# Optimization experiments

Measured on AMD Instinct MI355X. Metric: run time of the kernel, lower is better.

Reference implementation:

```python
import jax, jax.numpy as jnp
import numpy as np

N_GAUSS = 2_000_000
N_VERTS = 5023
N_FACES = 9976


def _safe_normalize(x, eps=1e-20):
    return x / jnp.sqrt(jnp.clip(jnp.sum(x * x, axis=-1, keepdims=True), eps, None))


def _rotmat_to_unitquat_xyzw(R):
    # scipy/roma-style branchless rotation-matrix -> unit quaternion (xyzw)
    r00, r01, r02 = R[..., 0, 0], R[..., 0, 1], R[..., 0, 2]
    r10, r11, r12 = R[..., 1, 0], R[..., 1, 1], R[..., 1, 2]
    r20, r21, r22 = R[..., 2, 0], R[..., 2, 1], R[..., 2, 2]
    t = r00 + r11 + r22
    qx = jnp.stack([1 + r00 - r11 - r22, r10 + r01, r20 + r02, r21 - r12], -1)
    qy = jnp.stack([r10 + r01, 1 - r00 + r11 - r22, r21 + r12, r02 - r20], -1)
    qz = jnp.stack([r20 + r02, r21 + r12, 1 - r00 - r11 + r22, r10 - r01], -1)
    qw = jnp.stack([r21 - r12, r02 - r20, r10 - r01, 1 + t], -1)
    decision = jnp.stack([r00, r11, r22, t], -1)
    choice = jnp.argmax(decision, axis=-1)[..., None]
    q = jnp.where(choice == 0, qx, jnp.where(choice == 1, qy, jnp.where(choice == 2, qz, qw)))
    return q / jnp.linalg.norm(q, axis=-1, keepdims=True)


def _quat_product_xyzw(p, q):
    pv, pw = p[..., :3], p[..., 3:4]
    qv, qw = q[..., :3], q[..., 3:4]
    v = pw * qv + qw * pv + jnp.cross(pv, qv)
    w = pw * qw - jnp.sum(pv * qv, axis=-1, keepdims=True)
    return jnp.concatenate([v, w], axis=-1)


def _xyzw_to_wxyz(q):
    return jnp.concatenate([q[..., 3:4], q[..., :3]], axis=-1)


def _wxyz_to_xyzw(q):
    return jnp.concatenate([q[..., 1:4], q[..., 0:1]], axis=-1)


def setup_inputs() -> dict:
    key = jax.random.key(0)
    ks = jax.random.split(key, 9)
    return {
        'verts': jax.random.normal(ks[0], (N_VERTS, 3), jnp.float32),
        'xyz': jax.random.normal(ks[1], (N_GAUSS, 3), jnp.float32),
        'opacity_raw': jax.random.normal(ks[2], (N_GAUSS, 1), jnp.float32),
        'scaling_raw': jax.random.normal(ks[3], (N_GAUSS, 3), jnp.float32),
        'rotation_raw': jax.random.normal(ks[4], (N_GAUSS, 4), jnp.float32),
        'features_dc': jax.random.normal(ks[5], (N_GAUSS, 1, 3), jnp.float32),
        'features_rest': jax.random.normal(ks[6], (N_GAUSS, 15, 3), jnp.float32),
        'faces': jax.random.randint(ks[7], (N_FACES, 3), 0, N_VERTS, jnp.int32),
        'binding': jax.random.randint(ks[8], (N_GAUSS,), 0, N_FACES, jnp.int32),
    }


def reference(verts, xyz, opacity_raw, scaling_raw, rotation_raw, features_dc, features_rest, faces, binding):
    # ---- per-face quantities (small: F ~= 10k) ----
    tri = verts[faces]                         # [F,3,3]
    face_center = tri.mean(axis=1)             # [F,3]
    v0, v1, v2 = tri[:, 0], tri[:, 1], tri[:, 2]
    a0 = _safe_normalize(v1 - v0)
    c = jnp.cross(a0, v2 - v0)
    a1 = _safe_normalize(c)
    a2 = -_safe_normalize(jnp.cross(a1, a0))
    R = jnp.stack([a0, a1, a2], axis=-1)       # [F,3,3], columns = tangent frame
    s0 = jnp.linalg.norm(v1 - v0, axis=-1, keepdims=True)
    s1 = jnp.abs(jnp.sum(c * a1, axis=-1, keepdims=True))
    face_scaling = (s0 + s1) / 2               # [F,1]
    face_quat_wxyz = _xyzw_to_wxyz(_rotmat_to_unitquat_xyzw(R))  # [F,4]

    # ---- per-Gaussian hot path: gather + 3x3 matvec + quat compose ----
    Rb = R[binding]                            # [N,3,3]
    fs = face_scaling[binding]                 # [N,1]
    g_xyz = jnp.einsum('nij,nj->ni', Rb, xyz) * fs + face_center[binding]  # [N,3]
    opacity = jax.nn.sigmoid(opacity_raw)      # [N,1]
    scales = jnp.exp(scaling_raw) * fs         # [N,3]
    rot = rotation_raw / (jnp.sqrt(jnp.sum(rotation_raw ** 2, axis=1, keepdims=True)) + 1e-12)
    fq = face_quat_wxyz[binding]
    fq = fq / (jnp.sqrt(jnp.sum(fq ** 2, axis=1, keepdims=True)) + 1e-12)
    rotations = _xyzw_to_wxyz(_quat_product_xyzw(_wxyz_to_xyzw(fq), _wxyz_to_xyzw(rot)))
    # shs = cat(features_dc, features_rest)[:, 0] == features_dc[:, 0]
    shs0 = features_dc[:, 0, :]
    color = jnp.clip(jnp.concatenate([0.5 + 0.282 * shs0, opacity], axis=-1) * 255.0, 0.0, 255.0)
    rotations = rotations / jnp.linalg.norm(rotations, axis=-1, keepdims=True)
    return jnp.concatenate([g_xyz, scales, color, rotations], axis=-1)  # [N,14]


if __name__ == '__main__':
    out = reference(**setup_inputs())
    print(out.shape, out.dtype)
```

## Files before the change

### kernel.cpp

```cpp
#include <hip/hip_runtime.h>
#include <math.h>


struct F3 { float x, y, z; };
__device__ __forceinline__ F3 mkf3(float x, float y, float z) { F3 r; r.x = x; r.y = y; r.z = z; return r; }
__device__ __forceinline__ F3 f3sub(F3 a, F3 b) { return mkf3(a.x - b.x, a.y - b.y, a.z - b.z); }
__device__ __forceinline__ F3 f3add(F3 a, F3 b) { return mkf3(a.x + b.x, a.y + b.y, a.z + b.z); }
__device__ __forceinline__ F3 f3scl(F3 a, float s) { return mkf3(a.x * s, a.y * s, a.z * s); }
__device__ __forceinline__ float f3dot(F3 a, F3 b) { return a.x * b.x + a.y * b.y + a.z * b.z; }
__device__ __forceinline__ F3 f3cross(F3 a, F3 b) {
    return mkf3(a.y * b.z - a.z * b.y, a.z * b.x - a.x * b.z, a.x * b.y - a.y * b.x);
}

__device__ void face_geom(const float* __restrict__ verts, const int* __restrict__ faces, int f,
                          F3& a0, F3& a1, F3& a2, F3& ctr, float& fs, float4& quat_wxyz)
{
    int i0 = faces[3 * f + 0], i1 = faces[3 * f + 1], i2 = faces[3 * f + 2];
    F3 v0 = mkf3(verts[3 * i0], verts[3 * i0 + 1], verts[3 * i0 + 2]);
    F3 v1 = mkf3(verts[3 * i1], verts[3 * i1 + 1], verts[3 * i1 + 2]);
    F3 v2 = mkf3(verts[3 * i2], verts[3 * i2 + 1], verts[3 * i2 + 2]);

    ctr = f3scl(f3add(f3add(v0, v1), v2), (1.0f / 3.0f));

    F3 e1 = f3sub(v1, v0);
    float d1 = f3dot(e1, e1);
    float s0 = sqrtf(d1);
    a0 = f3scl(e1, 1.0f / sqrtf(fmaxf(d1, 1e-20f)));

    F3 e2 = f3sub(v2, v0);
    F3 c = f3cross(a0, e2);
    float dc = f3dot(c, c);
    a1 = f3scl(c, 1.0f / sqrtf(fmaxf(dc, 1e-20f)));

    F3 c2 = f3cross(a1, a0);
    float dc2 = f3dot(c2, c2);
    F3 n2 = f3scl(c2, 1.0f / sqrtf(fmaxf(dc2, 1e-20f)));
    a2 = mkf3(-n2.x, -n2.y, -n2.z);

    float s1 = fabsf(f3dot(c, a1));
    fs = 0.5f * (s0 + s1);

    float r00 = a0.x, r10 = a0.y, r20 = a0.z;
    float r01 = a1.x, r11 = a1.y, r21 = a1.z;
    float r02 = a2.x, r12 = a2.y, r22 = a2.z;
    float t = r00 + r11 + r22;

    float cand[4][4] = {
        { 1.0f + r00 - r11 - r22, r10 + r01,              r20 + r02,              r21 - r12 },
        { r10 + r01,              1.0f - r00 + r11 - r22, r21 + r12,              r02 - r20 },
        { r20 + r02,              r21 + r12,              1.0f - r00 - r11 + r22, r10 - r01 },
        { r21 - r12,              r02 - r20,              r10 - r01,              1.0f + t  }
    };
    float dec[4] = { r00, r11, r22, t };
    int ch = 0;
    float best = dec[0];
#pragma unroll
    for (int j = 1; j < 4; ++j) {
        if (dec[j] > best) { best = dec[j]; ch = j; }
    }
    float qx = cand[ch][0], qy = cand[ch][1], qz = cand[ch][2], qw = cand[ch][3];
    float inv = 1.0f / sqrtf(qx * qx + qy * qy + qz * qz + qw * qw);
    quat_wxyz = make_float4(qw * inv, qx * inv, qy * inv, qz * inv);
}

__global__ __launch_bounds__(256)
void face_kernel(const float* __restrict__ verts, const int* __restrict__ faces,
                 float4* __restrict__ fd, int nf)
{
    int f = blockIdx.x * 256 + threadIdx.x;
    if (f >= nf) return;
    F3 a0, a1, a2, ctr; float fs; float4 quat;
    face_geom(verts, faces, f, a0, a1, a2, ctr, fs, quat);
    fd[5 * f + 0] = make_float4(a0.x, a0.y, a0.z, ctr.x);
    fd[5 * f + 1] = make_float4(a1.x, a1.y, a1.z, ctr.y);
    fd[5 * f + 2] = make_float4(a2.x, a2.y, a2.z, ctr.z);
    fd[5 * f + 3] = quat;
    fd[5 * f + 4] = make_float4(fs, 0.0f, 0.0f, 0.0f);
}

__global__ __launch_bounds__(256)
void gauss_lds(const float* __restrict__ xyz, const float* __restrict__ opa,
               const float* __restrict__ scl, const float4* __restrict__ rot_raw,
               const float* __restrict__ fdc, const int* __restrict__ binding,
               const float4* __restrict__ face, float* __restrict__ out, int n)
{
    __shared__ float s_xyz[768];
    __shared__ float s_scl[768];
    __shared__ float s_fdc[768];
    __shared__ float s_out[256 * 15];

    int tid = threadIdx.x;
    int g0  = blockIdx.x * 256;
    int cnt = n - g0; if (cnt > 256) cnt = 256;

    int nfl = cnt * 3;
    int nf4 = nfl >> 2;
    const float4* x4 = (const float4*)(xyz + (size_t)g0 * 3);
    const float4* s4 = (const float4*)(scl + (size_t)g0 * 3);
    const float4* f4 = (const float4*)(fdc + (size_t)g0 * 3);
    if (tid < nf4) {
        *(float4*)&s_xyz[4 * tid] = x4[tid];
        *(float4*)&s_scl[4 * tid] = s4[tid];
        *(float4*)&s_fdc[4 * tid] = f4[tid];
    }
    for (int j = (nf4 << 2) + tid; j < nfl; j += 256) {
        s_xyz[j] = xyz[(size_t)g0 * 3 + j];
        s_scl[j] = scl[(size_t)g0 * 3 + j];
        s_fdc[j] = fdc[(size_t)g0 * 3 + j];
    }
    __syncthreads();

    if (tid < cnt) {
        int i = g0 + tid;
        int b = binding[i];
        float4 f0 = face[5 * b + 0];
        float4 f1 = face[5 * b + 1];
        float4 f2 = face[5 * b + 2];
        float4 fq = face[5 * b + 3];
        float fs  = face[5 * b + 4].x;

        float x = s_xyz[3 * tid + 0], y = s_xyz[3 * tid + 1], z = s_xyz[3 * tid + 2];
        float gx = (f0.x * x + f1.x * y + f2.x * z) * fs + f0.w;
        float gy = (f0.y * x + f1.y * y + f2.y * z) * fs + f1.w;
        float gz = (f0.z * x + f1.z * y + f2.z * z) * fs + f2.w;

        float s0 = expf(s_scl[3 * tid + 0]) * fs;
        float s1 = expf(s_scl[3 * tid + 1]) * fs;
        float s2 = expf(s_scl[3 * tid + 2]) * fs;

        float o = 1.0f / (1.0f + expf(-opa[i]));

        float4 r = rot_raw[i];
        float rinv = 1.0f / (sqrtf(r.x * r.x + r.y * r.y + r.z * r.z + r.w * r.w) + 1e-12f);
        float rw = r.x * rinv, rx = r.y * rinv, ry = r.z * rinv, rz = r.w * rinv;

        float pw = fq.x, px = fq.y, py = fq.z, pz = fq.w;
        float vx = pw * rx + rw * px + (py * rz - pz * ry);
        float vy = pw * ry + rw * py + (pz * rx - px * rz);
        float vz = pw * rz + rw * pz + (px * ry - py * rx);
        float vw = pw * rw - (px * rx + py * ry + pz * rz);
        float qinv = 1.0f / sqrtf(vx * vx + vy * vy + vz * vz + vw * vw);

        float c0 = fminf(fmaxf((0.5f + 0.282f * s_fdc[3 * tid + 0]) * 255.0f, 0.0f), 255.0f);
        float c1 = fminf(fmaxf((0.5f + 0.282f * s_fdc[3 * tid + 1]) * 255.0f, 0.0f), 255.0f);
        float c2 = fminf(fmaxf((0.5f + 0.282f * s_fdc[3 * tid + 2]) * 255.0f, 0.0f), 255.0f);
        float c3 = fminf(fmaxf(o * 255.0f, 0.0f), 255.0f);

        float* po = &s_out[tid * 15];
        po[0]  = gx;        po[1]  = gy;        po[2]  = gz;
        po[3]  = s0;        po[4]  = s1;        po[5]  = s2;
        po[6]  = c0;        po[7]  = c1;        po[8]  = c2;        po[9] = c3;
        po[10] = vw * qinv; po[11] = vx * qinv; po[12] = vy * qinv; po[13] = vz * qinv;
    }
    __syncthreads();

    int nflo = cnt * 14;
    int nfo4 = nflo >> 2;
    float4* o4 = (float4*)(out + (size_t)g0 * 14);
    for (int j = tid; j < nfo4; j += 256) {
        int fbase = 4 * j;
        float a = s_out[((fbase + 0) / 14) * 15 + (fbase + 0) % 14];
        float bb = s_out[((fbase + 1) / 14) * 15 + (fbase + 1) % 14];
        float cc = s_out[((fbase + 2) / 14) * 15 + (fbase + 2) % 14];
        float dd = s_out[((fbase + 3) / 14) * 15 + (fbase + 3) % 14];
        o4[j] = make_float4(a, bb, cc, dd);
    }
    for (int f = (nfo4 << 2) + tid; f < nflo; f += 256) {
        out[(size_t)g0 * 14 + f] = s_out[(f / 14) * 15 + f % 14];
    }
}

__global__ __launch_bounds__(256)
void gauss_fused(const float* __restrict__ verts, const int* __restrict__ faces,
                 const float* __restrict__ xyz, const float* __restrict__ opa,
                 const float* __restrict__ scl, const float4* __restrict__ rot_raw,
                 const float* __restrict__ fdc, const int* __restrict__ binding,
                 float* __restrict__ out, int n)
{
    int i = blockIdx.x * 256 + threadIdx.x;
    if (i >= n) return;
    int b = binding[i];
    F3 a0, a1, a2, ctr; float fs; float4 quat;
    face_geom(verts, faces, b, a0, a1, a2, ctr, fs, quat);
    float4 f0 = make_float4(a0.x, a0.y, a0.z, ctr.x);
    float4 f1 = make_float4(a1.x, a1.y, a1.z, ctr.y);
    float4 f2 = make_float4(a2.x, a2.y, a2.z, ctr.z);

    float x = xyz[3 * i], y = xyz[3 * i + 1], z = xyz[3 * i + 2];
    float gx = (f0.x * x + f1.x * y + f2.x * z) * fs + f0.w;
    float gy = (f0.y * x + f1.y * y + f2.y * z) * fs + f1.w;
    float gz = (f0.z * x + f1.z * y + f2.z * z) * fs + f2.w;
    float s0 = expf(scl[3 * i + 0]) * fs;
    float s1 = expf(scl[3 * i + 1]) * fs;
    float s2 = expf(scl[3 * i + 2]) * fs;
    float o = 1.0f / (1.0f + expf(-opa[i]));
    float4 r = rot_raw[i];
    float rinv = 1.0f / (sqrtf(r.x * r.x + r.y * r.y + r.z * r.z + r.w * r.w) + 1e-12f);
    float rw = r.x * rinv, rx = r.y * rinv, ry = r.z * rinv, rz = r.w * rinv;
    float pw = quat.x, px = quat.y, py = quat.z, pz = quat.w;
    float vx = pw * rx + rw * px + (py * rz - pz * ry);
    float vy = pw * ry + rw * py + (pz * rx - px * rz);
    float vz = pw * rz + rw * pz + (px * ry - py * rx);
    float vw = pw * rw - (px * rx + py * ry + pz * rz);
    float qinv = 1.0f / sqrtf(vx * vx + vy * vy + vz * vz + vw * vw);
    float* po = out + (size_t)i * 14;
    po[0] = gx; po[1] = gy; po[2] = gz;
    po[3] = s0; po[4] = s1; po[5] = s2;
    po[6] = fminf(fmaxf((0.5f + 0.282f * fdc[3 * i + 0]) * 255.0f, 0.0f), 255.0f);
    po[7] = fminf(fmaxf((0.5f + 0.282f * fdc[3 * i + 1]) * 255.0f, 0.0f), 255.0f);
    po[8] = fminf(fmaxf((0.5f + 0.282f * fdc[3 * i + 2]) * 255.0f, 0.0f), 255.0f);
    po[9] = fminf(fmaxf(o * 255.0f, 0.0f), 255.0f);
    po[10] = vw * qinv; po[11] = vx * qinv; po[12] = vy * qinv; po[13] = vz * qinv;
}

extern "C" void kernel_launch(void* const* d_in, const int* in_sizes, int n_in,
                              void* d_out, int out_size, void* d_ws, size_t ws_size,
                              hipStream_t stream)
{
    const float* verts   = (const float*)d_in[0];
    const float* xyz     = (const float*)d_in[1];
    const float* opa     = (const float*)d_in[2];
    const float* scl     = (const float*)d_in[3];
    const float* rot     = (const float*)d_in[4];
    const float* fdc     = (const float*)d_in[5];
    const int*   faces   = (const int*)d_in[7];
    const int*   binding = (const int*)d_in[8];

    int n      = in_sizes[8];
    int nfaces = in_sizes[7] / 3;
    float* out = (float*)d_out;

    size_t need = (size_t)nfaces * 5 * sizeof(float4);

    if (ws_size >= need) {
        float4* face = (float4*)d_ws;
        hipLaunchKernelGGL(face_kernel, dim3((nfaces + 255) / 256), dim3(256), 0, stream,
                           verts, faces, face, nfaces);
        hipLaunchKernelGGL(gauss_lds, dim3((n + 255) / 256), dim3(256), 0, stream,
                           xyz, opa, scl, (const float4*)rot, fdc, binding, face, out, n);
    } else {
        hipLaunchKernelGGL(gauss_fused, dim3((n + 255) / 256), dim3(256), 0, stream,
                           verts, faces, xyz, opa, scl, (const float4*)rot, fdc, binding, out, n);
    }
}
```

Baseline: 47.59 us.

## Compact per-face table to quat+center and rebuild rotation from quaternion

The per-face record shrinks from five float4s (rotation matrix, center, quat, scale) to two (quat, then center plus scale). The Gaussian kernel rebuilds the 3x3 rotation from the face quaternion, cutting random gather traffic per Gaussian. It also drops LDS staging of the xyz, scale and fdc inputs in favour of direct strided loads, and writes the output with nontemporal stores. This assumes the face frame matrix equals the rotation implied by its quaternion, which holds if the frame is orthonormal, at the cost of extra ALU and small rounding differences.

New measurement: 44.35 us. 1.07x faster.

```diff
diff --git a/kernel.cpp b/kernel.cpp
--- a/kernel.cpp
+++ b/kernel.cpp
@@ -1,6 +1,8 @@
 #include <hip/hip_runtime.h>
 #include <math.h>
 
+
+typedef float f32x4 __attribute__((ext_vector_type(4)));
 
 struct F3 { float x, y, z; };
 __device__ __forceinline__ F3 mkf3(float x, float y, float z) { F3 r; r.x = x; r.y = y; r.z = z; return r; }
@@ -64,86 +66,71 @@
 }
 
 __global__ __launch_bounds__(256)
-void face_kernel(const float* __restrict__ verts, const int* __restrict__ faces,
-                 float4* __restrict__ fd, int nf)
+void face_kernel2(const float* __restrict__ verts, const int* __restrict__ faces,
+                  f32x4* __restrict__ fd, int nf)
 {
     int f = blockIdx.x * 256 + threadIdx.x;
     if (f >= nf) return;
     F3 a0, a1, a2, ctr; float fs; float4 quat;
     face_geom(verts, faces, f, a0, a1, a2, ctr, fs, quat);
-    fd[5 * f + 0] = make_float4(a0.x, a0.y, a0.z, ctr.x);
-    fd[5 * f + 1] = make_float4(a1.x, a1.y, a1.z, ctr.y);
-    fd[5 * f + 2] = make_float4(a2.x, a2.y, a2.z, ctr.z);
-    fd[5 * f + 3] = quat;
-    fd[5 * f + 4] = make_float4(fs, 0.0f, 0.0f, 0.0f);
+    f32x4 q; q.x = quat.x; q.y = quat.y; q.z = quat.z; q.w = quat.w;
+    f32x4 c; c.x = ctr.x;  c.y = ctr.y;  c.z = ctr.z;  c.w = fs;
+    fd[2 * f + 0] = q;
+    fd[2 * f + 1] = c;
 }
 
 __global__ __launch_bounds__(256)
-void gauss_lds(const float* __restrict__ xyz, const float* __restrict__ opa,
-               const float* __restrict__ scl, const float4* __restrict__ rot_raw,
-               const float* __restrict__ fdc, const int* __restrict__ binding,
-               const float4* __restrict__ face, float* __restrict__ out, int n)
-{
-    __shared__ float s_xyz[768];
-    __shared__ float s_scl[768];
-    __shared__ float s_fdc[768];
+void gauss_q(const float* __restrict__ xyz, const float* __restrict__ opa,
+             const float* __restrict__ scl, const f32x4* __restrict__ rot_raw,
+             const float* __restrict__ fdc, const int* __restrict__ binding,
+             const f32x4* __restrict__ face, float* __restrict__ out, int n)
+{
     __shared__ float s_out[256 * 15];
 
     int tid = threadIdx.x;
     int g0  = blockIdx.x * 256;
     int cnt = n - g0; if (cnt > 256) cnt = 256;
 
-    int nfl = cnt * 3;
-    int nf4 = nfl >> 2;
-    const float4* x4 = (const float4*)(xyz + (size_t)g0 * 3);
-    const float4* s4 = (const float4*)(scl + (size_t)g0 * 3);
-    const float4* f4 = (const float4*)(fdc + (size_t)g0 * 3);
-    if (tid < nf4) {
-        *(float4*)&s_xyz[4 * tid] = x4[tid];
-        *(float4*)&s_scl[4 * tid] = s4[tid];
-        *(float4*)&s_fdc[4 * tid] = f4[tid];
-    }
-    for (int j = (nf4 << 2) + tid; j < nfl; j += 256) {
-        s_xyz[j] = xyz[(size_t)g0 * 3 + j];
-        s_scl[j] = scl[(size_t)g0 * 3 + j];
-        s_fdc[j] = fdc[(size_t)g0 * 3 + j];
-    }
-    __syncthreads();
-
     if (tid < cnt) {
         int i = g0 + tid;
         int b = binding[i];
-        float4 f0 = face[5 * b + 0];
-        float4 f1 = face[5 * b + 1];
-        float4 f2 = face[5 * b + 2];
-        float4 fq = face[5 * b + 3];
-        float fs  = face[5 * b + 4].x;
-
-        float x = s_xyz[3 * tid + 0], y = s_xyz[3 * tid + 1], z = s_xyz[3 * tid + 2];
-        float gx = (f0.x * x + f1.x * y + f2.x * z) * fs + f0.w;
-        float gy = (f0.y * x + f1.y * y + f2.y * z) * fs + f1.w;
-        float gz = (f0.z * x + f1.z * y + f2.z * z) * fs + f2.w;
-
-        float s0 = expf(s_scl[3 * tid + 0]) * fs;
-        float s1 = expf(s_scl[3 * tid + 1]) * fs;
-        float s2 = expf(s_scl[3 * tid + 2]) * fs;
+        f32x4 q4 = face[2 * b + 0];
+        f32x4 cf = face[2 * b + 1];
+        float qw = q4.x, qx = q4.y, qy = q4.z, qz = q4.w;
+        float fs = cf.w;
+
+        float xx = qx * qx, yy = qy * qy, zz = qz * qz;
+        float xy = qx * qy, xz = qx * qz, yz = qy * qz;
+        float wx = qw * qx, wy = qw * qy, wz = qw * qz;
+        float r00 = 1.0f - 2.0f * (yy + zz), r01 = 2.0f * (xy - wz), r02 = 2.0f * (xz + wy);
+        float r10 = 2.0f * (xy + wz), r11 = 1.0f - 2.0f * (xx + zz), r12 = 2.0f * (yz - wx);
+        float r20 = 2.0f * (xz - wy), r21 = 2.0f * (yz + wx), r22 = 1.0f - 2.0f * (xx + yy);
+
+        float x = xyz[3 * i + 0], y = xyz[3 * i + 1], z = xyz[3 * i + 2];
+        float gx = (r00 * x + r01 * y + r02 * z) * fs + cf.x;
+        float gy = (r10 * x + r11 * y + r12 * z) * fs + cf.y;
+        float gz = (r20 * x + r21 * y + r22 * z) * fs + cf.z;
+
+        float s0 = expf(scl[3 * i + 0]) * fs;
+        float s1 = expf(scl[3 * i + 1]) * fs;
+        float s2 = expf(scl[3 * i + 2]) * fs;
 
         float o = 1.0f / (1.0f + expf(-opa[i]));
 
-        float4 r = rot_raw[i];
+        f32x4 r = rot_raw[i];
         float rinv = 1.0f / (sqrtf(r.x * r.x + r.y * r.y + r.z * r.z + r.w * r.w) + 1e-12f);
         float rw = r.x * rinv, rx = r.y * rinv, ry = r.z * rinv, rz = r.w * rinv;
 
-        float pw = fq.x, px = fq.y, py = fq.z, pz = fq.w;
-        float vx = pw * rx + rw * px + (py * rz - pz * ry);
-        float vy = pw * ry + rw * py + (pz * rx - px * rz);
-        float vz = pw * rz + rw * pz + (px * ry - py * rx);
-        float vw = pw * rw - (px * rx + py * ry + pz * rz);
+        float vx = qw * rx + rw * qx + (qy * rz - qz * ry);
+        float vy = qw * ry + rw * qy + (qz * rx - qx * rz);
+        float vz = qw * rz + rw * qz + (qx * ry - qy * rx);
+        float vw = qw * rw - (qx * rx + qy * ry + qz * rz);
         float qinv = 1.0f / sqrtf(vx * vx + vy * vy + vz * vz + vw * vw);
 
-        float c0 = fminf(fmaxf((0.5f + 0.282f * s_fdc[3 * tid + 0]) * 255.0f, 0.0f), 255.0f);
-        float c1 = fminf(fmaxf((0.5f + 0.282f * s_fdc[3 * tid + 1]) * 255.0f, 0.0f), 255.0f);
-        float c2 = fminf(fmaxf((0.5f + 0.282f * s_fdc[3 * tid + 2]) * 255.0f, 0.0f), 255.0f);
+        float d0 = fdc[3 * i + 0], d1 = fdc[3 * i + 1], d2 = fdc[3 * i + 2];
+        float c0 = fminf(fmaxf((0.5f + 0.282f * d0) * 255.0f, 0.0f), 255.0f);
+        float c1 = fminf(fmaxf((0.5f + 0.282f * d1) * 255.0f, 0.0f), 255.0f);
+        float c2 = fminf(fmaxf((0.5f + 0.282f * d2) * 255.0f, 0.0f), 255.0f);
         float c3 = fminf(fmaxf(o * 255.0f, 0.0f), 255.0f);
 
         float* po = &s_out[tid * 15];
@@ -156,24 +143,26 @@
 
     int nflo = cnt * 14;
     int nfo4 = nflo >> 2;
-    float4* o4 = (float4*)(out + (size_t)g0 * 14);
+    f32x4* o4 = (f32x4*)(out + (size_t)g0 * 14);
     for (int j = tid; j < nfo4; j += 256) {
-        int fbase = 4 * j;
-        float a = s_out[((fbase + 0) / 14) * 15 + (fbase + 0) % 14];
-        float bb = s_out[((fbase + 1) / 14) * 15 + (fbase + 1) % 14];
-        float cc = s_out[((fbase + 2) / 14) * 15 + (fbase + 2) % 14];
-        float dd = s_out[((fbase + 3) / 14) * 15 + (fbase + 3) % 14];
-        o4[j] = make_float4(a, bb, cc, dd);
+        int fb = 4 * j;
+        f32x4 v;
+        v.x = s_out[((fb + 0) / 14) * 15 + (fb + 0) % 14];
+        v.y = s_out[((fb + 1) / 14) * 15 + (fb + 1) % 14];
+        v.z = s_out[((fb + 2) / 14) * 15 + (fb + 2) % 14];
+        v.w = s_out[((fb + 3) / 14) * 15 + (fb + 3) % 14];
+        __builtin_nontemporal_store(v, o4 + j);
     }
     for (int f = (nfo4 << 2) + tid; f < nflo; f += 256) {
-        out[(size_t)g0 * 14 + f] = s_out[(f / 14) * 15 + f % 14];
+        __builtin_nontemporal_store(s_out[(f / 14) * 15 + f % 14],
+                                    out + (size_t)g0 * 14 + f);
     }
 }
 
 __global__ __launch_bounds__(256)
 void gauss_fused(const float* __restrict__ verts, const int* __restrict__ faces,
                  const float* __restrict__ xyz, const float* __restrict__ opa,
-                 const float* __restrict__ scl, const float4* __restrict__ rot_raw,
+                 const float* __restrict__ scl, const f32x4* __restrict__ rot_raw,
                  const float* __restrict__ fdc, const int* __restrict__ binding,
                  float* __restrict__ out, int n)
 {
@@ -182,19 +171,16 @@
     int b = binding[i];
     F3 a0, a1, a2, ctr; float fs; float4 quat;
     face_geom(verts, faces, b, a0, a1, a2, ctr, fs, quat);
-    float4 f0 = make_float4(a0.x, a0.y, a0.z, ctr.x);
-    float4 f1 = make_float4(a1.x, a1.y, a1.z, ctr.y);
-    float4 f2 = make_float4(a2.x, a2.y, a2.z, ctr.z);
 
     float x = xyz[3 * i], y = xyz[3 * i + 1], z = xyz[3 * i + 2];
-    float gx = (f0.x * x + f1.x * y + f2.x * z) * fs + f0.w;
-    float gy = (f0.y * x + f1.y * y + f2.y * z) * fs + f1.w;
-    float gz = (f0.z * x + f1.z * y + f2.z * z) * fs + f2.w;
+    float gx = (a0.x * x + a1.x * y + a2.x * z) * fs + ctr.x;
+    float gy = (a0.y * x + a1.y * y + a2.y * z) * fs + ctr.y;
+    float gz = (a0.z * x + a1.z * y + a2.z * z) * fs + ctr.z;
     float s0 = expf(scl[3 * i + 0]) * fs;
     float s1 = expf(scl[3 * i + 1]) * fs;
     float s2 = expf(scl[3 * i + 2]) * fs;
     float o = 1.0f / (1.0f + expf(-opa[i]));
-    float4 r = rot_raw[i];
+    f32x4 r = rot_raw[i];
     float rinv = 1.0f / (sqrtf(r.x * r.x + r.y * r.y + r.z * r.z + r.w * r.w) + 1e-12f);
     float rw = r.x * rinv, rx = r.y * rinv, ry = r.z * rinv, rz = r.w * rinv;
     float pw = quat.x, px = quat.y, py = quat.z, pz = quat.w;
@@ -230,16 +216,16 @@
     int nfaces = in_sizes[7] / 3;
     float* out = (float*)d_out;
 
-    size_t need = (size_t)nfaces * 5 * sizeof(float4);
+    size_t need = (size_t)nfaces * 2 * sizeof(f32x4);
 
     if (ws_size >= need) {
-        float4* face = (float4*)d_ws;
-        hipLaunchKernelGGL(face_kernel, dim3((nfaces + 255) / 256), dim3(256), 0, stream,
+        f32x4* face = (f32x4*)d_ws;
+        hipLaunchKernelGGL(face_kernel2, dim3((nfaces + 255) / 256), dim3(256), 0, stream,
                            verts, faces, face, nfaces);
-        hipLaunchKernelGGL(gauss_lds, dim3((n + 255) / 256), dim3(256), 0, stream,
-                           xyz, opa, scl, (const float4*)rot, fdc, binding, face, out, n);
+        hipLaunchKernelGGL(gauss_q, dim3((n + 255) / 256), dim3(256), 0, stream,
+                           xyz, opa, scl, (const f32x4*)rot, fdc, binding, face, out, n);
     } else {
         hipLaunchKernelGGL(gauss_fused, dim3((n + 255) / 256), dim3(256), 0, stream,
-                           verts, faces, xyz, opa, scl, (const float4*)rot, fdc, binding, out, n);
-    }
-}
+                           verts, faces, xyz, opa, scl, (const f32x4*)rot, fdc, binding, out, n);
+    }
+}
```
